# Kernel tuning notes

Measured on AMD Instinct MI355X. Metric: run time of the kernel, lower is better.

The kernel has to match this reference:

```python
import jax, jax.numpy as jnp
import numpy as np

N, R, K = 4, 16384, 96


def setup_inputs() -> dict:
    key = jax.random.key(0)
    k1, k2, k3 = jax.random.split(key, 3)
    rgbs = jax.random.uniform(k1, (N, R, K, 3), dtype=jnp.float32)
    sigmas = jax.random.normal(k2, (N, R, K, 1), dtype=jnp.float32)
    # depths must be monotonically increasing along K (ray sample depths in [0.5, 3.5])
    depths = jnp.sort(0.5 + 3.0 * jax.random.uniform(k3, (N, R, K, 1), dtype=jnp.float32), axis=2)
    return {"rgbs": rgbs, "sigmas": sigmas, "depths": depths}


def reference(rgbs, sigmas, depths):
    # Default rendering_options: use_max_depth=False, no_dist=False,
    # use_mid_point=True, clamp_mode='mipnerf', last_back=False,
    # normalize_rgb=False, normalize_depth=True, clip_depth=True, white_back=False.
    deltas = depths[:, :, 1:] - depths[:, :, :-1]                  # [N,R,K-1,1]
    # midpoint averaging
    rgbs_m = 0.5 * (rgbs[:, :, :-1] + rgbs[:, :, 1:])              # [N,R,K-1,3]
    sigmas_m = 0.5 * (sigmas[:, :, :-1] + sigmas[:, :, 1:])        # [N,R,K-1,1]
    depths_m = 0.5 * (depths[:, :, :-1] + depths[:, :, 1:])        # [N,R,K-1,1]
    # mipnerf clamp: softplus(sigma - 1)
    sig = jax.nn.softplus(sigmas_m - 1.0)
    alphas = 1.0 - jnp.exp(-deltas * sig)                          # [N,R,K-1,1]
    # transmittance via exclusive cumprod along the sample axis
    alphas_shifted = jnp.concatenate(
        [jnp.ones_like(alphas[:, :, :1]), 1.0 - alphas + 1e-10], axis=-2)
    trans = jnp.cumprod(alphas_shifted, axis=-2)[:, :, :-1]        # [N,R,K-1,1]
    weights = alphas * trans                                       # [N,R,K-1,1]
    weights_sum = weights.sum(axis=2)                              # [N,R,1]
    composite_rgb = jnp.sum(weights * rgbs_m, axis=-2)             # [N,R,3]
    composite_depth = jnp.sum(weights * depths_m, axis=-2)         # [N,R,1]
    # normalize_depth=True
    composite_depth = composite_depth / weights_sum
    # clip_depth=True
    composite_depth = jnp.nan_to_num(composite_depth, nan=jnp.inf)
    composite_depth = jnp.clip(composite_depth, depths_m.min(), depths_m.max())
    composite_rgb = composite_rgb * 2.0 - 1.0
    return composite_rgb, composite_depth, weights
```

## Files before the change

kernel.cpp:

```cpp
#include <hip/hip_runtime.h>
#include <math.h>

#define NRAYS     65536
#define RGB_OFF   0
#define DEPTH_OFF (NRAYS * 3)
#define W_OFF     (NRAYS * 4)

typedef float f4u __attribute__((ext_vector_type(4), aligned(4)));
typedef float f2u __attribute__((ext_vector_type(2), aligned(4)));

#define DPPF(oldv, x, ctrl)                                                    \
    __int_as_float(__builtin_amdgcn_update_dpp(                                \
        __float_as_int(oldv), __float_as_int(x), (ctrl), 0xF, 0xF, false))

__device__ __forceinline__ float one_minus_alpha(float x, float delta) {
    const float L2E = 1.44269504088896340736f;
    float xl = x * L2E;
    float l2 = (x > 20.0f) ? xl
                           : __builtin_amdgcn_logf(1.0f + __builtin_amdgcn_exp2f(xl));
    return __builtin_amdgcn_exp2f(-delta * l2);
}

__global__ __launch_bounds__(256) void integrate_kernel(
    const float* __restrict__ rgbs,
    const float* __restrict__ sigmas,
    const float* __restrict__ depths,
    float* __restrict__ out)
{
    const int t    = threadIdx.x;
    const int l    = t & 15;
    const int ray  = blockIdx.x * 16 + (t >> 4);
    const bool full = (l < 15);

    const float* db = depths + ray * 96  + 6 * l;
    const float* sb = sigmas + ray * 96  + 6 * l;
    const float* rb = rgbs   + ray * 288 + 18 * l;

    float2 e0 = *(const float2*)(db);
    float2 e1 = *(const float2*)(db + 2);
    float2 e2 = *(const float2*)(db + 4);
    float  d6 = full ? db[6] : 0.f;
    float2 f0 = *(const float2*)(sb);
    float2 f1 = *(const float2*)(sb + 2);
    float2 f2v = *(const float2*)(sb + 4);
    float  s6 = full ? sb[6] : 0.f;
    float2 c0 = *(const float2*)(rb);
    float2 c1 = *(const float2*)(rb + 2);
    float2 c2 = *(const float2*)(rb + 4);
    float2 c3 = *(const float2*)(rb + 6);
    float2 c4 = *(const float2*)(rb + 8);
    float2 c5 = *(const float2*)(rb + 10);
    float2 c6 = *(const float2*)(rb + 12);
    float2 c7 = *(const float2*)(rb + 14);
    float2 c8 = *(const float2*)(rb + 16);
    float2 c9 = full ? *(const float2*)(rb + 18) : float2{0.f, 0.f};
    float  r20 = full ? rb[20] : 0.f;

    const float D[7] = {e0.x, e0.y, e1.x, e1.y, e2.x, e2.y, d6};
    const float S[7] = {f0.x, f0.y, f1.x, f1.y, f2v.x, f2v.y, s6};
    const float R[7] = {c0.x, c1.y, c3.x, c4.y, c6.x, c7.y, c9.x};
    const float G[7] = {c0.y, c2.x, c3.y, c5.x, c6.y, c8.x, c9.y};
    const float B[7] = {c1.x, c2.y, c4.x, c5.y, c7.x, c8.y, r20};

    float u[6];
    float Tloc = 1.0f;
    float Sw = 0.f, Sd = 0.f, Sr = 0.f, Sg = 0.f, Sbv = 0.f;

#define DO_IV(I)                                                      \
    { float delta = D[(I)+1] - D[I];                                  \
      float x = 0.5f * (S[I] + S[(I)+1]) - 1.0f;                      \
      float e = one_minus_alpha(x, delta);                            \
      float uu = (1.0f - e) * Tloc;                                   \
      Tloc *= e + 1e-10f;                                             \
      u[I] = uu;                                                      \
      Sw  += uu;                                                      \
      Sd  += uu * (0.5f * (D[I] + D[(I)+1]));                         \
      Sr  += uu * (0.5f * (R[I] + R[(I)+1]));                         \
      Sg  += uu * (0.5f * (G[I] + G[(I)+1]));                         \
      Sbv += uu * (0.5f * (B[I] + B[(I)+1])); }

    DO_IV(0) DO_IV(1) DO_IV(2) DO_IV(3) DO_IV(4)
    if (full) { DO_IV(5) } else { u[5] = 0.f; }
#undef DO_IV

    float incl = Tloc;
    incl *= DPPF(1.0f, incl, 0x111);
    incl *= DPPF(1.0f, incl, 0x112);
    incl *= DPPF(1.0f, incl, 0x114);
    incl *= DPPF(1.0f, incl, 0x118);
    float Tin = DPPF(1.0f, incl, 0x111);

    Sw *= Tin; Sd *= Tin; Sr *= Tin; Sg *= Tin; Sbv *= Tin;

#define RED(v)                         \
    v += DPPF(0.f, v, 0x111);          \
    v += DPPF(0.f, v, 0x112);          \
    v += DPPF(0.f, v, 0x114);          \
    v += DPPF(0.f, v, 0x118);
    RED(Sw) RED(Sd) RED(Sr) RED(Sg) RED(Sbv)
#undef RED

    float lo0 = 0.5f * (D[0] + D[1]);
    float lo  = DPPF(0.f, lo0, 0x11F);

    float* wout = out + W_OFF + ray * 95 + 6 * l;
    f4u v4 = { Tin * u[0], Tin * u[1], Tin * u[2], Tin * u[3] };
    *(f4u*)wout = v4;
    if (full) {
        f2u v2 = { Tin * u[4], Tin * u[5] };
        *(f2u*)(wout + 4) = v2;
    } else {
        wout[4] = Tin * u[4];
    }

    if (l == 15) {
        out[RGB_OFF + ray * 3 + 0] = 2.f * Sr  - 1.f;
        out[RGB_OFF + ray * 3 + 1] = 2.f * Sg  - 1.f;
        out[RGB_OFF + ray * 3 + 2] = 2.f * Sbv - 1.f;
        float dv = Sd / Sw;
        float hi = 0.5f * (D[4] + D[5]);
        dv = fmaxf(fminf(dv, hi), lo);
        out[DEPTH_OFF + ray] = dv;
    }
}

extern "C" void kernel_launch(void* const* d_in, const int* in_sizes, int n_in,
                              void* d_out, int out_size, void* d_ws, size_t ws_size,
                              hipStream_t stream) {
    const float* rgbs   = (const float*)d_in[0];
    const float* sigmas = (const float*)d_in[1];
    const float* depths = (const float*)d_in[2];
    float* out = (float*)d_out;

    integrate_kernel<<<NRAYS / 16, 256, 0, stream>>>(rgbs, sigmas, depths, out);
}
```

Baseline: 157.6 us.

## Stage block inputs into LDS via direct global-to-LDS loads

Each block first copies its 16 rays of depths, sigmas and rgbs into shared memory with 16-byte global_load_lds instructions, which gives fully coalesced wide loads. After a barrier, threads read their strided per-lane segments from LDS. Because reads now come from padded LDS, the per-lane boundary guards go away. The cost is a block-wide barrier, extra LDS traffic and footprint (about 30 KB per block), and less overlap between loading and computing.

```diff
diff --git a/kernel.cpp b/kernel.cpp
--- a/kernel.cpp
+++ b/kernel.cpp
@@ -5,6 +5,12 @@
 #define RGB_OFF   0
 #define DEPTH_OFF (NRAYS * 3)
 #define W_OFF     (NRAYS * 4)
+
+#define RPB 16
+#define SHD_OFF 0
+#define SHS_OFF 1540
+#define SHR_OFF 3080
+#define SH_TOTAL 7696
 
 typedef float f4u __attribute__((ext_vector_type(4), aligned(4)));
 typedef float f2u __attribute__((ext_vector_type(2), aligned(4)));
@@ -21,43 +27,72 @@
     return __builtin_amdgcn_exp2f(-delta * l2);
 }
 
+__device__ __forceinline__ void gload_lds16(const float* g, float* l) {
+    __builtin_amdgcn_global_load_lds(
+        (const __attribute__((address_space(1))) void*)g,
+        (__attribute__((address_space(3))) void*)l, 16, 0, 0);
+}
+
 __global__ __launch_bounds__(256) void integrate_kernel(
     const float* __restrict__ rgbs,
     const float* __restrict__ sigmas,
     const float* __restrict__ depths,
     float* __restrict__ out)
 {
-    const int t    = threadIdx.x;
-    const int l    = t & 15;
-    const int ray  = blockIdx.x * 16 + (t >> 4);
+    __shared__ float sh[SH_TOTAL];
+
+    const int t   = threadIdx.x;
+    const int w   = t >> 6;
+    const int l64 = t & 63;
+    const int blk = blockIdx.x;
+
+    {
+        const float* gd = depths + (size_t)blk * (RPB * 96);
+        const float* gs = sigmas + (size_t)blk * (RPB * 96);
+        const float* gr = rgbs   + (size_t)blk * (RPB * 288);
+        for (int c = w; c < 30; c += 4) {
+            const float* src;
+            float* dst;
+            if (c < 6)       { src = gd + c * 256;        dst = sh + SHD_OFF + c * 256; }
+            else if (c < 12) { src = gs + (c - 6) * 256;  dst = sh + SHS_OFF + (c - 6) * 256; }
+            else             { src = gr + (c - 12) * 256; dst = sh + SHR_OFF + (c - 12) * 256; }
+            gload_lds16(src + l64 * 4, dst + l64 * 4);
+        }
+    }
+    __builtin_amdgcn_s_waitcnt(0x0F70);
+    __syncthreads();
+
+    const int rb_ = t >> 4;
+    const int l   = t & 15;
+    const int ray = blk * RPB + rb_;
     const bool full = (l < 15);
 
-    const float* db = depths + ray * 96  + 6 * l;
-    const float* sb = sigmas + ray * 96  + 6 * l;
-    const float* rb = rgbs   + ray * 288 + 18 * l;
+    const float* db = sh + SHD_OFF + rb_ * 96  + 6 * l;
+    const float* sp = sh + SHS_OFF + rb_ * 96  + 6 * l;
+    const float* rp = sh + SHR_OFF + rb_ * 288 + 18 * l;
 
     float2 e0 = *(const float2*)(db);
     float2 e1 = *(const float2*)(db + 2);
     float2 e2 = *(const float2*)(db + 4);
-    float  d6 = full ? db[6] : 0.f;
-    float2 f0 = *(const float2*)(sb);
-    float2 f1 = *(const float2*)(sb + 2);
-    float2 f2v = *(const float2*)(sb + 4);
-    float  s6 = full ? sb[6] : 0.f;
-    float2 c0 = *(const float2*)(rb);
-    float2 c1 = *(const float2*)(rb + 2);
-    float2 c2 = *(const float2*)(rb + 4);
-    float2 c3 = *(const float2*)(rb + 6);
-    float2 c4 = *(const float2*)(rb + 8);
-    float2 c5 = *(const float2*)(rb + 10);
-    float2 c6 = *(const float2*)(rb + 12);
-    float2 c7 = *(const float2*)(rb + 14);
-    float2 c8 = *(const float2*)(rb + 16);
-    float2 c9 = full ? *(const float2*)(rb + 18) : float2{0.f, 0.f};
-    float  r20 = full ? rb[20] : 0.f;
+    float2 e3 = *(const float2*)(db + 6);
+    float2 f0 = *(const float2*)(sp);
+    float2 f1 = *(const float2*)(sp + 2);
+    float2 f2v = *(const float2*)(sp + 4);
+    float2 f3 = *(const float2*)(sp + 6);
+    float2 c0 = *(const float2*)(rp);
+    float2 c1 = *(const float2*)(rp + 2);
+    float2 c2 = *(const float2*)(rp + 4);
+    float2 c3 = *(const float2*)(rp + 6);
+    float2 c4 = *(const float2*)(rp + 8);
+    float2 c5 = *(const float2*)(rp + 10);
+    float2 c6 = *(const float2*)(rp + 12);
+    float2 c7 = *(const float2*)(rp + 14);
+    float2 c8 = *(const float2*)(rp + 16);
+    float2 c9 = *(const float2*)(rp + 18);
+    float  r20 = rp[20];
 
-    const float D[7] = {e0.x, e0.y, e1.x, e1.y, e2.x, e2.y, d6};
-    const float S[7] = {f0.x, f0.y, f1.x, f1.y, f2v.x, f2v.y, s6};
+    const float D[7] = {e0.x, e0.y, e1.x, e1.y, e2.x, e2.y, e3.x};
+    const float S[7] = {f0.x, f0.y, f1.x, f1.y, f2v.x, f2v.y, f3.x};
     const float R[7] = {c0.x, c1.y, c3.x, c4.y, c6.x, c7.y, c9.x};
     const float G[7] = {c0.y, c2.x, c3.y, c5.x, c6.y, c8.x, c9.y};
     const float B[7] = {c1.x, c2.y, c4.x, c5.y, c7.x, c8.y, r20};
@@ -103,7 +138,7 @@
     float lo0 = 0.5f * (D[0] + D[1]);
     float lo  = DPPF(0.f, lo0, 0x11F);
 
-    float* wout = out + W_OFF + ray * 95 + 6 * l;
+    float* wout = out + W_OFF + (size_t)ray * 95 + 6 * l;
     f4u v4 = { Tin * u[0], Tin * u[1], Tin * u[2], Tin * u[3] };
     *(f4u*)wout = v4;
     if (full) {
@@ -132,5 +167,5 @@
     const float* depths = (const float*)d_in[2];
     float* out = (float*)d_out;
 
-    integrate_kernel<<<NRAYS / 16, 256, 0, stream>>>(rgbs, sigmas, depths, out);
+    integrate_kernel<<<NRAYS / RPB, 256, 0, stream>>>(rgbs, sigmas, depths, out);
 }
```

New measurement: 157.2 us. No clear change (-0.3%).
